# Kernel tuning notes

Hardware: AMD Instinct MI355X
Metric: run time of the kernel (lower is better)

## Reference

```python
import jax, jax.numpy as jnp
import numpy as np


def setup_inputs() -> dict:
    key = jax.random.key(0)
    k1, k2, k3, k4 = jax.random.split(key, 4)
    N, E, C_in, C_out = 100000, 1600000, 256, 128
    x = jax.random.normal(k1, (N, C_in), dtype=jnp.float32)
    edge_index = jax.random.randint(k2, (2, E), 0, N, dtype=jnp.int64)
    W = jax.random.normal(k3, (C_in, C_out), dtype=jnp.float32) * 0.05
    b = jax.random.normal(k4, (C_out,), dtype=jnp.float32) * 0.05
    return {"x": x, "edge_index": edge_index, "W": W, "b": b}


def reference(x, edge_index, W, b):
    # GCNConv (PyG defaults): add self-loops, symmetric normalization,
    # linear transform, scatter-sum aggregation, bias; then ReLU (norm=None).
    N = x.shape[0]
    loops = jnp.arange(N, dtype=edge_index.dtype)
    src = jnp.concatenate([edge_index[0], loops])  # [E+N] message sources (x_j)
    dst = jnp.concatenate([edge_index[1], loops])  # [E+N] aggregation targets

    deg = jax.ops.segment_sum(jnp.ones_like(dst, dtype=x.dtype), dst, num_segments=N)
    deg_inv_sqrt = jnp.where(deg > 0, jax.lax.rsqrt(jnp.maximum(deg, 1.0)), 0.0)
    norm = deg_inv_sqrt[src] * deg_inv_sqrt[dst]  # [E+N]

    h = x @ W                                      # [N, C_out]
    msg = h[src] * norm[:, None]                   # [E+N, C_out] gather + scale
    out = jax.ops.segment_sum(msg, dst, num_segments=N) + b  # scatter-add
    return jax.nn.relu(out)
```

## Files before the change

### kernel.cpp

```cpp
#include <hip/hip_runtime.h>


__device__ __forceinline__ unsigned short f2bf(float f) {
  unsigned int u = __float_as_uint(f);
  u += 0x7FFFu + ((u >> 16) & 1u);
  return (unsigned short)(u >> 16);
}
__device__ __forceinline__ float bf0(unsigned int u) { return __uint_as_float(u << 16); }
__device__ __forceinline__ float bf1(unsigned int u) { return __uint_as_float(u & 0xFFFF0000u); }

__global__ __launch_bounds__(256) void k_gemm_scatter(
    const float* __restrict__ x, const float* __restrict__ W,
    unsigned short* __restrict__ h, int N,
    const int* __restrict__ src, const int* __restrict__ dst,
    unsigned int* __restrict__ cnt, int* __restrict__ srcs, int E,
    int gemmB, int scatB)
{
  __shared__ float xst[32][36];
  __shared__ float wsm[32][132];

  const int id = blockIdx.x;
  bool isGemm;
  int idx;
  if (scatB == 2 * gemmB) {
    if (id % 3 == 0) { isGemm = true;  idx = id / 3; }
    else             { isGemm = false; idx = id - 1 - id / 3; }
  } else {
    isGemm = id < gemmB;
    idx = isGemm ? id : id - gemmB;
  }

  const int tid = threadIdx.x;

  if (!isGemm) {
    if (idx < scatB) {
      int e = idx * 256 + tid;
      if (e < E) {
        int d = dst[e];
        int pos = (int)atomicAdd(&cnt[d], 1u);
        if (pos < 64) srcs[((size_t)d << 6) + pos] = src[e];
      }
    }
    return;
  }
  if (idx >= gemmB) return;

  const int row0 = idx * 32;
  const int cg = tid & 31;
  const int rg = tid >> 5;
  float acc[4][4] = {};

  for (int k0 = 0; k0 < 256; k0 += 32) {
    {
      int r = tid >> 3;
      int c = (tid & 7) * 4;
      int row = row0 + r; if (row >= N) row = N - 1;
      const float4 v = *(const float4*)(x + (size_t)row * 256 + k0 + c);
      xst[c + 0][r] = v.x;
      xst[c + 1][r] = v.y;
      xst[c + 2][r] = v.z;
      xst[c + 3][r] = v.w;
    }
    #pragma unroll
    for (int i = 0; i < 4; i++) {
      int widx = tid + i * 256;
      int wr = widx >> 5;
      int wc = (widx & 31) * 4;
      *(float4*)&wsm[wr][wc] = *(const float4*)(W + (size_t)(k0 + wr) * 128 + wc);
    }
    __syncthreads();
    #pragma unroll
    for (int kk = 0; kk < 32; kk++) {
      const float4 wv = *(const float4*)&wsm[kk][cg * 4];
      const float4 xv = *(const float4*)&xst[kk][rg * 4];
      const float xa[4] = {xv.x, xv.y, xv.z, xv.w};
      #pragma unroll
      for (int j = 0; j < 4; j++) {
        acc[j][0] = fmaf(xa[j], wv.x, acc[j][0]);
        acc[j][1] = fmaf(xa[j], wv.y, acc[j][1]);
        acc[j][2] = fmaf(xa[j], wv.z, acc[j][2]);
        acc[j][3] = fmaf(xa[j], wv.w, acc[j][3]);
      }
    }
    __syncthreads();
  }

  #pragma unroll
  for (int j = 0; j < 4; j++) {
    const int row = row0 + rg * 4 + j;
    if (row < N) {
      unsigned int lo = (unsigned int)f2bf(acc[j][0]) | ((unsigned int)f2bf(acc[j][1]) << 16);
      unsigned int hi = (unsigned int)f2bf(acc[j][2]) | ((unsigned int)f2bf(acc[j][3]) << 16);
      *(uint2*)(h + (size_t)row * 128 + cg * 4) = make_uint2(lo, hi);
    }
  }
}

__global__ __launch_bounds__(256) void k_aggr(
    const unsigned short* __restrict__ h, const int* __restrict__ srcs,
    const unsigned int* __restrict__ cnt,
    const float* __restrict__ b, float* __restrict__ out, int N)
{
  const int wid = (int)(((size_t)blockIdx.x * 256 + threadIdx.x) >> 6);
  if (wid >= N) return;
  const int lane = threadIdx.x & 63;
  const int eg = lane >> 4;
  const int cl = lane & 15;
  const int deg = min((int)cnt[wid], 64);
  const int m = deg + 1;
  const size_t coff = (size_t)(cl << 3);
  const size_t lbase = (size_t)wid << 6;

  float a0 = 0.f, a1 = 0.f, a2 = 0.f, a3 = 0.f, a4 = 0.f, a5 = 0.f, a6 = 0.f, a7 = 0.f;

  for (int base = 0; base < m; base += 64) {
    const int kk = min(64, m - base);
    const int slot = base + lane;
    int sidx = wid;
    if (slot < deg) sidx = srcs[lbase + slot];
    const float sd = rsqrtf((float)(cnt[sidx] + 1u));
    int j = 0;
    for (; j + 8 <= kk; j += 8) {
      const int s0 = __shfl(sidx, j + eg, 64);
      const int s1 = __shfl(sidx, j + 4 + eg, 64);
      const float d0 = __shfl(sd, j + eg, 64);
      const float d1 = __shfl(sd, j + 4 + eg, 64);
      const uint4 v0 = *(const uint4*)(h + ((size_t)s0 << 7) + coff);
      const uint4 v1 = *(const uint4*)(h + ((size_t)s1 << 7) + coff);
      a0 = fmaf(bf0(v0.x), d0, a0); a1 = fmaf(bf1(v0.x), d0, a1);
      a2 = fmaf(bf0(v0.y), d0, a2); a3 = fmaf(bf1(v0.y), d0, a3);
      a4 = fmaf(bf0(v0.z), d0, a4); a5 = fmaf(bf1(v0.z), d0, a5);
      a6 = fmaf(bf0(v0.w), d0, a6); a7 = fmaf(bf1(v0.w), d0, a7);
      a0 = fmaf(bf0(v1.x), d1, a0); a1 = fmaf(bf1(v1.x), d1, a1);
      a2 = fmaf(bf0(v1.y), d1, a2); a3 = fmaf(bf1(v1.y), d1, a3);
      a4 = fmaf(bf0(v1.z), d1, a4); a5 = fmaf(bf1(v1.z), d1, a5);
      a6 = fmaf(bf0(v1.w), d1, a6); a7 = fmaf(bf1(v1.w), d1, a7);
    }
    for (; j < kk; j += 4) {
      const int s0 = __shfl(sidx, j + eg, 64);
      const float d0 = __shfl(sd, j + eg, 64);
      if (j + eg < kk) {
        const uint4 v0 = *(const uint4*)(h + ((size_t)s0 << 7) + coff);
        a0 = fmaf(bf0(v0.x), d0, a0); a1 = fmaf(bf1(v0.x), d0, a1);
        a2 = fmaf(bf0(v0.y), d0, a2); a3 = fmaf(bf1(v0.y), d0, a3);
        a4 = fmaf(bf0(v0.z), d0, a4); a5 = fmaf(bf1(v0.z), d0, a5);
        a6 = fmaf(bf0(v0.w), d0, a6); a7 = fmaf(bf1(v0.w), d0, a7);
      }
    }
  }

  a0 += __shfl_xor(a0, 16, 64); a0 += __shfl_xor(a0, 32, 64);
  a1 += __shfl_xor(a1, 16, 64); a1 += __shfl_xor(a1, 32, 64);
  a2 += __shfl_xor(a2, 16, 64); a2 += __shfl_xor(a2, 32, 64);
  a3 += __shfl_xor(a3, 16, 64); a3 += __shfl_xor(a3, 32, 64);
  a4 += __shfl_xor(a4, 16, 64); a4 += __shfl_xor(a4, 32, 64);
  a5 += __shfl_xor(a5, 16, 64); a5 += __shfl_xor(a5, 32, 64);
  a6 += __shfl_xor(a6, 16, 64); a6 += __shfl_xor(a6, 32, 64);
  a7 += __shfl_xor(a7, 16, 64); a7 += __shfl_xor(a7, 32, 64);

  if (lane < 32) {
    const float dn = rsqrtf((float)m);
    const int hi = lane >> 4;
    const int c0 = ((lane & 15) << 3) + (hi << 2);
    const float4 bb = *(const float4*)(b + c0);
    const float r0 = hi ? a4 : a0;
    const float r1 = hi ? a5 : a1;
    const float r2 = hi ? a6 : a2;
    const float r3 = hi ? a7 : a3;
    float4 o;
    o.x = fmaxf(fmaf(dn, r0, bb.x), 0.f);
    o.y = fmaxf(fmaf(dn, r1, bb.y), 0.f);
    o.z = fmaxf(fmaf(dn, r2, bb.z), 0.f);
    o.w = fmaxf(fmaf(dn, r3, bb.w), 0.f);
    *(float4*)(out + ((size_t)wid << 7) + c0) = o;
  }
}

extern "C" void kernel_launch(void* const* d_in, const int* in_sizes, int n_in,
                              void* d_out, int out_size, void* d_ws, size_t ws_size,
                              hipStream_t stream)
{
  const float* x  = (const float*)d_in[0];
  const int* ei   = (const int*)d_in[1];
  const float* W  = (const float*)d_in[2];
  const float* b  = (const float*)d_in[3];
  float* out = (float*)d_out;

  const int Cout = in_sizes[3];
  const int Cin  = in_sizes[2] / Cout;
  const int N    = in_sizes[0] / Cin;
  const int E    = in_sizes[1] / 2;

  const int* src = ei;
  const int* dst = ei + E;

  char* p = (char*)d_ws;
  size_t off = 0;
  auto alloc = [&](size_t bytes) { char* q = p + off; off = (off + bytes + 255) & ~(size_t)255; return q; };
  unsigned int* cnt = (unsigned int*)alloc((size_t)N * 4);
  int* srcs         = (int*)alloc((size_t)N * 64 * 4);
  unsigned short* h = (unsigned short*)alloc((size_t)N * Cout * 2);

  const int gemmB = (N + 31) / 32;
  const int scatB = (E + 255) / 256;

  hipMemsetAsync(cnt, 0, (size_t)N * 4, stream);
  k_gemm_scatter<<<gemmB + scatB, 256, 0, stream>>>(x, W, h, N,
                                                    src, dst, cnt, srcs, E,
                                                    gemmB, scatB);
  k_aggr<<<(N + 3) / 4, 256, 0, stream>>>(h, srcs, cnt, b, out, N);
}
```

Before: 334.0 us.

## Compute GEMM with split-bf16 MFMA instead of FP32 FMA

Replaces the scalar FP32 FMA tile loop in the fused GEMM/scatter kernel with MFMA 16x16x32 bf16 instructions. A and B are each split into hi+lo bf16 parts and three MFMAs are issued to keep near-FP32 accuracy. W is pre-split and swizzled into a blob by a new small prep kernel, and x is split on the fly into swizzled shared memory. This moves the GEMM from vector ALUs to matrix cores, at the cost of one extra launch, conversion work and scalar 2-byte output stores.

```diff
diff --git a/kernel.cpp b/kernel.cpp
--- a/kernel.cpp
+++ b/kernel.cpp
@@ -1,23 +1,44 @@
 #include <hip/hip_runtime.h>
 
+
+typedef __attribute__((ext_vector_type(8))) short bf16x8;
+typedef __attribute__((ext_vector_type(4))) float f32x4;
 
 __device__ __forceinline__ unsigned short f2bf(float f) {
   unsigned int u = __float_as_uint(f);
   u += 0x7FFFu + ((u >> 16) & 1u);
   return (unsigned short)(u >> 16);
 }
+__device__ __forceinline__ float bfval(unsigned short h) {
+  return __uint_as_float(((unsigned int)h) << 16);
+}
 __device__ __forceinline__ float bf0(unsigned int u) { return __uint_as_float(u << 16); }
 __device__ __forceinline__ float bf1(unsigned int u) { return __uint_as_float(u & 0xFFFF0000u); }
 
+__global__ __launch_bounds__(256) void k_wprep(
+    const float* __restrict__ W, unsigned short* __restrict__ blob)
+{
+  int g = blockIdx.x * 256 + threadIdx.x;
+  if (g >= 256 * 128) return;
+  int k = g >> 7, c = g & 127;
+  float w = W[g];
+  unsigned short hi = f2bf(w);
+  unsigned short lo = f2bf(w - bfval(hi));
+  int q = k >> 5, kk = k & 31;
+  unsigned lin = (unsigned)(c * 64 + kk * 2);
+  unsigned swz = lin ^ (((unsigned)(c & 7)) << 4);
+  blob[(q * 16384 + swz) >> 1] = hi;
+  blob[(q * 16384 + 8192 + swz) >> 1] = lo;
+}
+
 __global__ __launch_bounds__(256) void k_gemm_scatter(
-    const float* __restrict__ x, const float* __restrict__ W,
+    const float* __restrict__ x, const unsigned char* __restrict__ wblob,
     unsigned short* __restrict__ h, int N,
     const int* __restrict__ src, const int* __restrict__ dst,
     unsigned int* __restrict__ cnt, int* __restrict__ srcs, int E,
     int gemmB, int scatB)
 {
-  __shared__ float xst[32][36];
-  __shared__ float wsm[32][132];
+  __shared__ __align__(16) unsigned char smem[20480];
 
   const int id = blockIdx.x;
   bool isGemm;
@@ -46,52 +67,66 @@
   if (idx >= gemmB) return;
 
   const int row0 = idx * 32;
-  const int cg = tid & 31;
-  const int rg = tid >> 5;
-  float acc[4][4] = {};
-
-  for (int k0 = 0; k0 < 256; k0 += 32) {
+  const int lane = tid & 63;
+  const int wv = tid >> 6;
+  const int mb = wv & 1;
+  const int nb = wv >> 1;
+
+  f32x4 acc[4] = {};
+
+  const int ar = tid >> 3;
+  const int akk0 = (tid & 7) * 4;
+  int arow = row0 + ar; if (arow >= N) arow = N - 1;
+  const unsigned aaddr = ((unsigned)(ar * 64 + akk0 * 2)) ^ (((unsigned)(ar & 7)) << 4);
+
+  const int rr = 16 * mb + (lane & 15);
+  const unsigned aoff = ((unsigned)(rr * 64 + (lane >> 4) * 16)) ^ (((unsigned)(rr & 7)) << 4);
+
+  for (int q = 0; q < 8; ++q) {
     {
-      int r = tid >> 3;
-      int c = (tid & 7) * 4;
-      int row = row0 + r; if (row >= N) row = N - 1;
-      const float4 v = *(const float4*)(x + (size_t)row * 256 + k0 + c);
-      xst[c + 0][r] = v.x;
-      xst[c + 1][r] = v.y;
-      xst[c + 2][r] = v.z;
-      xst[c + 3][r] = v.w;
-    }
+      const float4 v = *(const float4*)(x + (size_t)arow * 256 + q * 32 + akk0);
+      unsigned short h0 = f2bf(v.x), h1 = f2bf(v.y), h2 = f2bf(v.z), h3 = f2bf(v.w);
+      unsigned short l0 = f2bf(v.x - bfval(h0));
+      unsigned short l1 = f2bf(v.y - bfval(h1));
+      unsigned short l2 = f2bf(v.z - bfval(h2));
+      unsigned short l3 = f2bf(v.w - bfval(h3));
+      *(uint2*)(smem + 16384 + aaddr) =
+          make_uint2((unsigned)h0 | ((unsigned)h1 << 16), (unsigned)h2 | ((unsigned)h3 << 16));
+      *(uint2*)(smem + 18432 + aaddr) =
+          make_uint2((unsigned)l0 | ((unsigned)l1 << 16), (unsigned)l2 | ((unsigned)l3 << 16));
+    }
+    {
+      const uint4* gb = (const uint4*)(wblob + (size_t)q * 16384);
+      uint4* sb = (uint4*)smem;
+      uint4 t0 = gb[tid], t1 = gb[tid + 256], t2 = gb[tid + 512], t3 = gb[tid + 768];
+      sb[tid] = t0; sb[tid + 256] = t1; sb[tid + 512] = t2; sb[tid + 768] = t3;
+    }
+    __syncthreads();
+    {
+      const bf16x8 ah = *(const bf16x8*)(smem + 16384 + aoff);
+      const bf16x8 al = *(const bf16x8*)(smem + 18432 + aoff);
+      #pragma unroll
+      for (int nf = 0; nf < 4; ++nf) {
+        const int c = 64 * nb + 16 * nf + (lane & 15);
+        const unsigned boff =
+            ((unsigned)(c * 64 + (lane >> 4) * 16)) ^ (((unsigned)(c & 7)) << 4);
+        const bf16x8 bh = *(const bf16x8*)(smem + boff);
+        const bf16x8 bl = *(const bf16x8*)(smem + 8192 + boff);
+        acc[nf] = __builtin_amdgcn_mfma_f32_16x16x32_bf16(ah, bh, acc[nf], 0, 0, 0);
+        acc[nf] = __builtin_amdgcn_mfma_f32_16x16x32_bf16(ah, bl, acc[nf], 0, 0, 0);
+        acc[nf] = __builtin_amdgcn_mfma_f32_16x16x32_bf16(al, bh, acc[nf], 0, 0, 0);
+      }
+    }
+    __syncthreads();
+  }
+
+  #pragma unroll
+  for (int nf = 0; nf < 4; ++nf) {
+    const int col = 64 * nb + 16 * nf + (lane & 15);
     #pragma unroll
-    for (int i = 0; i < 4; i++) {
-      int widx = tid + i * 256;
-      int wr = widx >> 5;
-      int wc = (widx & 31) * 4;
-      *(float4*)&wsm[wr][wc] = *(const float4*)(W + (size_t)(k0 + wr) * 128 + wc);
-    }
-    __syncthreads();
-    #pragma unroll
-    for (int kk = 0; kk < 32; kk++) {
-      const float4 wv = *(const float4*)&wsm[kk][cg * 4];
-      const float4 xv = *(const float4*)&xst[kk][rg * 4];
-      const float xa[4] = {xv.x, xv.y, xv.z, xv.w};
-      #pragma unroll
-      for (int j = 0; j < 4; j++) {
-        acc[j][0] = fmaf(xa[j], wv.x, acc[j][0]);
-        acc[j][1] = fmaf(xa[j], wv.y, acc[j][1]);
-        acc[j][2] = fmaf(xa[j], wv.z, acc[j][2]);
-        acc[j][3] = fmaf(xa[j], wv.w, acc[j][3]);
-      }
-    }
-    __syncthreads();
-  }
-
-  #pragma unroll
-  for (int j = 0; j < 4; j++) {
-    const int row = row0 + rg * 4 + j;
-    if (row < N) {
-      unsigned int lo = (unsigned int)f2bf(acc[j][0]) | ((unsigned int)f2bf(acc[j][1]) << 16);
-      unsigned int hi = (unsigned int)f2bf(acc[j][2]) | ((unsigned int)f2bf(acc[j][3]) << 16);
-      *(uint2*)(h + (size_t)row * 128 + cg * 4) = make_uint2(lo, hi);
+    for (int r = 0; r < 4; ++r) {
+      const int row = row0 + 16 * mb + 4 * (lane >> 4) + r;
+      if (row < N) h[(size_t)row * 128 + col] = f2bf(acc[nf][r]);
     }
   }
 }
@@ -200,12 +235,14 @@
   unsigned int* cnt = (unsigned int*)alloc((size_t)N * 4);
   int* srcs         = (int*)alloc((size_t)N * 64 * 4);
   unsigned short* h = (unsigned short*)alloc((size_t)N * Cout * 2);
+  unsigned short* wblob = (unsigned short*)alloc(8 * 16384);
 
   const int gemmB = (N + 31) / 32;
   const int scatB = (E + 255) / 256;
 
+  k_wprep<<<128, 256, 0, stream>>>(W, wblob);
   hipMemsetAsync(cnt, 0, (size_t)N * 4, stream);
-  k_gemm_scatter<<<gemmB + scatB, 256, 0, stream>>>(x, W, h, N,
+  k_gemm_scatter<<<gemmB + scatB, 256, 0, stream>>>(x, (const unsigned char*)wblob, h, N,
                                                     src, dst, cnt, srcs, E,
                                                     gemmB, scatB);
   k_aggr<<<(N + 3) / 4, 256, 0, stream>>>(h, srcs, cnt, b, out, N);
```

After: 327.4 us. 1.02x faster.
